# Optimization experiments

Measured on AMD Instinct MI355X. Metric: run time of the kernel, lower is better.

## Reference

```python
import jax, jax.numpy as jnp
import numpy as np

N_WORDS = 30000
EMB_DIM = 784          # must be a perfect square
MAT_DIM = 28           # sqrt(784)
BATCH = 256
SEQ_LEN = 64


def setup_inputs() -> dict:
    key = jax.random.key(0)
    k_sent, k_w = jax.random.split(key)
    # token ids in [1, N_WORDS]; row 0 of the table is the identity (neutral) element
    sent = jax.random.randint(k_sent, (BATCH, SEQ_LEN), 1, N_WORDS + 1, dtype=jnp.int64) \
        if jax.config.jax_enable_x64 else \
        jax.random.randint(k_sent, (BATCH, SEQ_LEN), 1, N_WORDS + 1, dtype=jnp.int32)
    # 'identity' initialization: N(0, 0.1) + flattened identity, prepended identity neutral row
    eye_flat = jnp.eye(MAT_DIM, dtype=jnp.float32).reshape(-1)        # [784]
    init_w = 0.1 * jax.random.normal(k_w, (N_WORDS, EMB_DIM), dtype=jnp.float32) + eye_flat
    lookup_weight = jnp.concatenate([eye_flat[None, :], init_w], axis=0)  # [N_WORDS+1, 784]
    return {"sent": sent, "lookup_weight": lookup_weight}


def reference(sent, lookup_weight):
    # CMOW: embedding lookup, reshape each word vector to a 28x28 matrix,
    # then a left-to-right chain of matrix products over the sequence.
    B, S = sent.shape
    mats = lookup_weight[sent].reshape(B, S, MAT_DIM, MAT_DIM)   # [B, S, 28, 28]
    # Log-depth parallel prefix product over the sequence axis (matmul is associative).
    prods = jax.lax.associative_scan(lambda a, b: a @ b, mats, axis=1)
    cur_emb = prods[:, -1]                                       # [B, 28, 28]
    return cur_emb.reshape(-1, EMB_DIM)                          # [B, 784]
```

## Files before the change

kernel.cpp:

```cpp
#include <hip/hip_runtime.h>
#include <hip/hip_bf16.h>


typedef float f32x4 __attribute__((ext_vector_type(4)));

namespace {
constexpr int MD  = 28;
constexpr int EMB = 784;
constexpr int SEQ = 64;
constexpr int BATCH = 256;
constexpr int SEG = 8;
constexpr int LEN = 8;
}

__device__ __forceinline__ void kloop(const float* __restrict__ A,
                                      const float* __restrict__ B,
                                      int r0, int c0,
                                      f32x4& a0, f32x4& a1, f32x4& a2, f32x4& a3) {
  f32x4 z = {0.f, 0.f, 0.f, 0.f};
  a0 = a1 = a2 = a3 = z;
#pragma unroll
  for (int k = 0; k < MD; ++k) {
    f32x4 rv = *reinterpret_cast<const f32x4*>(A + k * MD + r0);
    f32x4 mv = *reinterpret_cast<const f32x4*>(B + k * MD + c0);
    a0 += rv[0] * mv;
    a1 += rv[1] * mv;
    a2 += rv[2] * mv;
    a3 += rv[3] * mv;
  }
}

__device__ __forceinline__ void store_T(float* __restrict__ D, int r0, int c0,
                                        const f32x4& a0, const f32x4& a1,
                                        const f32x4& a2, const f32x4& a3) {
#pragma unroll
  for (int cc = 0; cc < 4; ++cc) {
    f32x4 v = { a0[cc], a1[cc], a2[cc], a3[cc] };
    *reinterpret_cast<f32x4*>(D + (c0 + cc) * MD + r0) = v;
  }
}

__device__ __forceinline__ void store_N(float* __restrict__ D, int r0, int c0,
                                        const f32x4& a0, const f32x4& a1,
                                        const f32x4& a2, const f32x4& a3) {
  *reinterpret_cast<f32x4*>(D + (r0 + 0) * MD + c0) = a0;
  *reinterpret_cast<f32x4*>(D + (r0 + 1) * MD + c0) = a1;
  *reinterpret_cast<f32x4*>(D + (r0 + 2) * MD + c0) = a2;
  *reinterpret_cast<f32x4*>(D + (r0 + 3) * MD + c0) = a3;
}

__global__ __launch_bounds__(64, 1)
void w2m_partial(const int* __restrict__ sent,
                 const float* __restrict__ W,
                 float* __restrict__ ws) {
  __shared__ __align__(16) float Ms[2][EMB];
  __shared__ __align__(16) float Rt[2][EMB];

  const int blk   = blockIdx.x;
  const int batch = blk >> 3;
  const int seg   = blk & 7;
  const int lane  = threadIdx.x;
  const bool act  = lane < 49;
  const int i = lane / 7, j = lane % 7;
  const int r0 = 4 * i, c0 = 4 * j;
  const int* srow = sent + batch * SEQ + seg * LEN;

  f32x4 sA0, sA1, sA2, sA3;
  f32x4 sB0, sB1, sB2, sB3;

  auto gload = [&](int t, f32x4& v0, f32x4& v1, f32x4& v2, f32x4& v3) {
    const f32x4* src = reinterpret_cast<const f32x4*>(W + (size_t)srow[t] * EMB);
    v0 = src[lane];
    v1 = src[64 + lane];
    v2 = src[128 + lane];
    if (lane < 4) v3 = src[192 + lane];
  };
  auto lwrite = [&](float* dst, const f32x4& v0, const f32x4& v1,
                    const f32x4& v2, const f32x4& v3) {
    f32x4* d = reinterpret_cast<f32x4*>(dst);
    d[lane] = v0;
    d[64 + lane] = v1;
    d[128 + lane] = v2;
    if (lane < 4) d[192 + lane] = v3;
  };

  gload(0, sA0, sA1, sA2, sA3);
  if (act) {
#pragma unroll
    for (int cc = 0; cc < 4; ++cc) {
      int d = (c0 + cc) - r0;
      f32x4 v = { d == 0 ? 1.f : 0.f, d == 1 ? 1.f : 0.f,
                  d == 2 ? 1.f : 0.f, d == 3 ? 1.f : 0.f };
      *reinterpret_cast<f32x4*>(&Rt[0][(c0 + cc) * MD + r0]) = v;
    }
  }
  lwrite(Ms[0], sA0, sA1, sA2, sA3);
  gload(1, sB0, sB1, sB2, sB3);

  f32x4 a0, a1, a2, a3;
#pragma unroll 1
  for (int tp = 0; tp < LEN; tp += 2) {
    lwrite(Ms[1], sB0, sB1, sB2, sB3);
    if (tp + 2 < LEN) gload(tp + 2, sA0, sA1, sA2, sA3);
    if (act) {
      kloop(Rt[0], Ms[0], r0, c0, a0, a1, a2, a3);
      store_T(Rt[1], r0, c0, a0, a1, a2, a3);
    }
    if (tp + 2 < LEN) lwrite(Ms[0], sA0, sA1, sA2, sA3);
    if (tp + 3 < LEN) gload(tp + 3, sB0, sB1, sB2, sB3);
    if (act) {
      kloop(Rt[1], Ms[1], r0, c0, a0, a1, a2, a3);
      if (tp + 1 < LEN - 1) {
        store_T(Rt[0], r0, c0, a0, a1, a2, a3);
      } else {
        float* pb = ws + (size_t)(batch * SEG + seg) * EMB;
        if (seg & 1) store_N(pb, r0, c0, a0, a1, a2, a3);
        else         store_T(pb, r0, c0, a0, a1, a2, a3);
      }
    }
  }
}

__global__ __launch_bounds__(256, 1)
void w2m_combine(const float* __restrict__ ws, float* __restrict__ out) {
  __shared__ __align__(16) float P[SEG][EMB];
  __shared__ __align__(16) float Q[4][EMB];
  __shared__ __align__(16) float Rl[2][EMB];

  const int batch = blockIdx.x;
  const int tid   = threadIdx.x;
  const int w     = tid >> 6;
  const int lane  = tid & 63;
  const bool act  = lane < 49;
  const int i = lane / 7, j = lane % 7;
  const int r0 = 4 * i, c0 = 4 * j;

  {
    const f32x4* src = reinterpret_cast<const f32x4*>(ws + (size_t)batch * SEG * EMB);
    f32x4* dst = reinterpret_cast<f32x4*>(&P[0][0]);
    for (int u = tid; u < SEG * EMB / 4; u += 256) dst[u] = src[u];
  }
  __syncthreads();

  f32x4 a0, a1, a2, a3;
  if (act) {
    kloop(P[2 * w], P[2 * w + 1], r0, c0, a0, a1, a2, a3);
    if (w & 1) store_N(Q[w], r0, c0, a0, a1, a2, a3);
    else       store_T(Q[w], r0, c0, a0, a1, a2, a3);
  }
  __syncthreads();
  if (w < 2 && act) {
    kloop(Q[2 * w], Q[2 * w + 1], r0, c0, a0, a1, a2, a3);
    if (w & 1) store_N(Rl[w], r0, c0, a0, a1, a2, a3);
    else       store_T(Rl[w], r0, c0, a0, a1, a2, a3);
  }
  __syncthreads();
  if (w == 0 && act) {
    kloop(Rl[0], Rl[1], r0, c0, a0, a1, a2, a3);
    store_N(out + (size_t)batch * EMB, r0, c0, a0, a1, a2, a3);
  }
}

extern "C" void kernel_launch(void* const* d_in, const int* in_sizes, int n_in,
                              void* d_out, int out_size, void* d_ws, size_t ws_size,
                              hipStream_t stream) {
  const int*   sent = (const int*)d_in[0];
  const float* W    = (const float*)d_in[1];
  float*       out  = (float*)d_out;
  float*       ws   = (float*)d_ws;
  (void)in_sizes; (void)n_in; (void)out_size; (void)ws_size;

  w2m_partial<<<BATCH * SEG, 64, 0, stream>>>(sent, W, ws);
  w2m_combine<<<BATCH, 256, 0, stream>>>(ws, out);
}
```

Before: 141.5 us.

## Use split-bf16 MFMA for per-segment matrix chain products

Replaces the scalar FP32 per-segment chain multiply with 32x32x16 bf16 MFMA instructions. Each fp32 operand is split into a high and low bf16 part and three products (hh, hl, lh) are summed to approximate fp32 accuracy. The running product is kept in registers and re-staged through a small padded LDS tile, while the next word matrix is prefetched straight from global memory into registers. It pads the 28x28 matrices to 32x32, which wastes some MFMA work, and the dropped lo*lo term adds rounding error that compounds over the chain.

After: 178.2 us. 1.26x slower.

```diff
diff --git a/kernel.cpp b/kernel.cpp
--- a/kernel.cpp
+++ b/kernel.cpp
@@ -2,7 +2,10 @@
 #include <hip/hip_bf16.h>
 
 
-typedef float f32x4 __attribute__((ext_vector_type(4)));
+typedef float f32x2  __attribute__((ext_vector_type(2)));
+typedef float f32x4  __attribute__((ext_vector_type(4)));
+typedef float f32x16 __attribute__((ext_vector_type(16)));
+typedef short bf16x8 __attribute__((ext_vector_type(8)));
 
 namespace {
 constexpr int MD  = 28;
@@ -11,7 +14,144 @@
 constexpr int BATCH = 256;
 constexpr int SEG = 8;
 constexpr int LEN = 8;
-}
+constexpr int LDP = 34;
+}
+
+__device__ __forceinline__ bf16x8 mkfrag(uint32_t w0, uint32_t w1,
+                                         uint32_t w2, uint32_t w3) {
+  union { uint32_t w[4]; bf16x8 b; } u;
+  u.w[0] = w0; u.w[1] = w1; u.w[2] = w2; u.w[3] = w3;
+  return u.b;
+}
+
+__device__ __forceinline__ void split8(const float* x, bf16x8& hi, bf16x8& lo) {
+  uint32_t H[4], L[4];
+#pragma unroll
+  for (int p = 0; p < 4; ++p) {
+    float x0 = x[2 * p], x1 = x[2 * p + 1];
+    uint32_t h0 = __float_as_uint(x0) & 0xffff0000u;
+    uint32_t h1 = __float_as_uint(x1) & 0xffff0000u;
+    float l0 = x0 - __uint_as_float(h0);
+    float l1 = x1 - __uint_as_float(h1);
+    H[p] = (h0 >> 16) | h1;
+    L[p] = (__float_as_uint(l0) >> 16) | (__float_as_uint(l1) & 0xffff0000u);
+  }
+  hi = mkfrag(H[0], H[1], H[2], H[3]);
+  lo = mkfrag(L[0], L[1], L[2], L[3]);
+}
+
+__global__ __launch_bounds__(64, 2)
+void w2m_partial_mfma(const int* __restrict__ sent,
+                      const float* __restrict__ W,
+                      float* __restrict__ ws) {
+  __shared__ __align__(16) float RL[32][LDP];
+
+  const int blk   = blockIdx.x;
+  const int batch = blk >> 3;
+  const int seg   = blk & 7;
+  const int lane  = threadIdx.x;
+  const int n = lane & 31;
+  const int h = lane >> 5;
+  const int* srow = sent + batch * SEQ + seg * LEN;
+
+  auto loadB = [&](const float* __restrict__ Mt, float* b) {
+#pragma unroll
+    for (int K = 0; K < 2; ++K)
+#pragma unroll
+      for (int e = 0; e < 8; ++e) {
+        int k = 16 * K + 8 * h + e;
+        int km = k < MD ? k : 0;
+        int nm = n < MD ? n : 0;
+        float t = Mt[km * MD + nm];
+        b[K * 8 + e] = (k < MD && n < MD) ? t : 0.f;
+      }
+  };
+
+  float a[16];
+  {
+    const float* __restrict__ M0 = W + (size_t)srow[0] * EMB;
+    const int m = n;
+#pragma unroll
+    for (int K = 0; K < 2; ++K)
+#pragma unroll
+      for (int u = 0; u < 2; ++u) {
+        int k0 = 16 * K + 8 * h + 4 * u;
+        f32x4 v = {0.f, 0.f, 0.f, 0.f};
+        if (m < MD && k0 < MD)
+          v = *reinterpret_cast<const f32x4*>(M0 + m * MD + k0);
+        a[K * 8 + 4 * u + 0] = v[0];
+        a[K * 8 + 4 * u + 1] = v[1];
+        a[K * 8 + 4 * u + 2] = v[2];
+        a[K * 8 + 4 * u + 3] = v[3];
+      }
+  }
+
+  float b_nxt[16];
+  loadB(W + (size_t)srow[1] * EMB, b_nxt);
+
+  f32x16 d;
+#pragma unroll
+  for (int t = 1; t < LEN; ++t) {
+    float b_cur[16];
+#pragma unroll
+    for (int q = 0; q < 16; ++q) b_cur[q] = b_nxt[q];
+    if (t < LEN - 1) loadB(W + (size_t)srow[t + 1] * EMB, b_nxt);
+
+    bf16x8 ah0, al0, ah1, al1, bh0, bl0, bh1, bl1;
+    split8(a,      ah0, al0);
+    split8(a + 8,  ah1, al1);
+    split8(b_cur,     bh0, bl0);
+    split8(b_cur + 8, bh1, bl1);
+
+#pragma unroll
+    for (int q = 0; q < 16; ++q) d[q] = 0.f;
+    d = __builtin_amdgcn_mfma_f32_32x32x16_bf16(ah0, bh0, d, 0, 0, 0);
+    d = __builtin_amdgcn_mfma_f32_32x32x16_bf16(ah0, bl0, d, 0, 0, 0);
+    d = __builtin_amdgcn_mfma_f32_32x32x16_bf16(al0, bh0, d, 0, 0, 0);
+    d = __builtin_amdgcn_mfma_f32_32x32x16_bf16(ah1, bh1, d, 0, 0, 0);
+    d = __builtin_amdgcn_mfma_f32_32x32x16_bf16(ah1, bl1, d, 0, 0, 0);
+    d = __builtin_amdgcn_mfma_f32_32x32x16_bf16(al1, bh1, d, 0, 0, 0);
+
+    if (t < LEN - 1) {
+#pragma unroll
+      for (int e = 0; e < 16; ++e) {
+        int r = (e & 3) + 8 * (e >> 2) + 4 * h;
+        RL[r][n] = d[e];
+      }
+      const int m = n;
+#pragma unroll
+      for (int K = 0; K < 2; ++K)
+#pragma unroll
+        for (int u = 0; u < 4; ++u) {
+          int k0 = 16 * K + 8 * h + 2 * u;
+          f32x2 v = *reinterpret_cast<const f32x2*>(&RL[m][k0]);
+          a[K * 8 + 2 * u + 0] = v[0];
+          a[K * 8 + 2 * u + 1] = v[1];
+        }
+    }
+  }
+
+  float* pb = ws + (size_t)(batch * SEG + seg) * EMB;
+  if (n < MD) {
+    if ((seg & 1) == 0) {
+#pragma unroll
+      for (int q = 0; q < 4; ++q) {
+        int rbase = 8 * q + 4 * h;
+        if (rbase < MD) {
+          f32x4 v = { d[4 * q], d[4 * q + 1], d[4 * q + 2], d[4 * q + 3] };
+          *reinterpret_cast<f32x4*>(pb + n * MD + rbase) = v;
+        }
+      }
+    } else {
+#pragma unroll
+      for (int e = 0; e < 16; ++e) {
+        int r = (e & 3) + 8 * (e >> 2) + 4 * h;
+        if (r < MD) pb[r * MD + n] = d[e];
+      }
+    }
+  }
+}
+
 
 __device__ __forceinline__ void kloop(const float* __restrict__ A,
                                       const float* __restrict__ B,
@@ -47,78 +187,6 @@
   *reinterpret_cast<f32x4*>(D + (r0 + 1) * MD + c0) = a1;
   *reinterpret_cast<f32x4*>(D + (r0 + 2) * MD + c0) = a2;
   *reinterpret_cast<f32x4*>(D + (r0 + 3) * MD + c0) = a3;
-}
-
-__global__ __launch_bounds__(64, 1)
-void w2m_partial(const int* __restrict__ sent,
-                 const float* __restrict__ W,
-                 float* __restrict__ ws) {
-  __shared__ __align__(16) float Ms[2][EMB];
-  __shared__ __align__(16) float Rt[2][EMB];
-
-  const int blk   = blockIdx.x;
-  const int batch = blk >> 3;
-  const int seg   = blk & 7;
-  const int lane  = threadIdx.x;
-  const bool act  = lane < 49;
-  const int i = lane / 7, j = lane % 7;
-  const int r0 = 4 * i, c0 = 4 * j;
-  const int* srow = sent + batch * SEQ + seg * LEN;
-
-  f32x4 sA0, sA1, sA2, sA3;
-  f32x4 sB0, sB1, sB2, sB3;
-
-  auto gload = [&](int t, f32x4& v0, f32x4& v1, f32x4& v2, f32x4& v3) {
-    const f32x4* src = reinterpret_cast<const f32x4*>(W + (size_t)srow[t] * EMB);
-    v0 = src[lane];
-    v1 = src[64 + lane];
-    v2 = src[128 + lane];
-    if (lane < 4) v3 = src[192 + lane];
-  };
-  auto lwrite = [&](float* dst, const f32x4& v0, const f32x4& v1,
-                    const f32x4& v2, const f32x4& v3) {
-    f32x4* d = reinterpret_cast<f32x4*>(dst);
-    d[lane] = v0;
-    d[64 + lane] = v1;
-    d[128 + lane] = v2;
-    if (lane < 4) d[192 + lane] = v3;
-  };
-
-  gload(0, sA0, sA1, sA2, sA3);
-  if (act) {
-#pragma unroll
-    for (int cc = 0; cc < 4; ++cc) {
-      int d = (c0 + cc) - r0;
-      f32x4 v = { d == 0 ? 1.f : 0.f, d == 1 ? 1.f : 0.f,
-                  d == 2 ? 1.f : 0.f, d == 3 ? 1.f : 0.f };
-      *reinterpret_cast<f32x4*>(&Rt[0][(c0 + cc) * MD + r0]) = v;
-    }
-  }
-  lwrite(Ms[0], sA0, sA1, sA2, sA3);
-  gload(1, sB0, sB1, sB2, sB3);
-
-  f32x4 a0, a1, a2, a3;
-#pragma unroll 1
-  for (int tp = 0; tp < LEN; tp += 2) {
-    lwrite(Ms[1], sB0, sB1, sB2, sB3);
-    if (tp + 2 < LEN) gload(tp + 2, sA0, sA1, sA2, sA3);
-    if (act) {
-      kloop(Rt[0], Ms[0], r0, c0, a0, a1, a2, a3);
-      store_T(Rt[1], r0, c0, a0, a1, a2, a3);
-    }
-    if (tp + 2 < LEN) lwrite(Ms[0], sA0, sA1, sA2, sA3);
-    if (tp + 3 < LEN) gload(tp + 3, sB0, sB1, sB2, sB3);
-    if (act) {
-      kloop(Rt[1], Ms[1], r0, c0, a0, a1, a2, a3);
-      if (tp + 1 < LEN - 1) {
-        store_T(Rt[0], r0, c0, a0, a1, a2, a3);
-      } else {
-        float* pb = ws + (size_t)(batch * SEG + seg) * EMB;
-        if (seg & 1) store_N(pb, r0, c0, a0, a1, a2, a3);
-        else         store_T(pb, r0, c0, a0, a1, a2, a3);
-      }
-    }
-  }
 }
 
 __global__ __launch_bounds__(256, 1)
@@ -170,6 +238,6 @@
   float*       ws   = (float*)d_ws;
   (void)in_sizes; (void)n_in; (void)out_size; (void)ws_size;
 
-  w2m_partial<<<BATCH * SEG, 64, 0, stream>>>(sent, W, ws);
+  w2m_partial_mfma<<<BATCH * SEG, 64, 0, stream>>>(sent, W, ws);
   w2m_combine<<<BATCH, 256, 0, stream>>>(ws, out);
 }
```
